# Kernel tuning notes

Hardware: AMD Instinct MI355X
Metric: run time of the kernel (lower is better)

Reference implementation:

```python
import jax, jax.numpy as jnp
import numpy as np
import math

B, S, E, H = 4, 2048, 512, 8
D = E // H

def setup_inputs() -> dict:
    key = jax.random.key(0)
    ks = jax.random.split(key, 12)
    inp = {
        'query': jax.random.normal(ks[0], (B, S, E), jnp.float32),
        'key': jax.random.normal(ks[1], (B, S, E), jnp.float32),
        'value': jax.random.normal(ks[2], (B, S, E), jnp.float32),
        'mask': jnp.ones((B, S), jnp.int32),
        'position_bias': jax.random.normal(ks[3], (H, S, S), jnp.float32) * 0.02,
        'Wq': jax.random.normal(ks[4], (E, E), jnp.float32) * 0.02,
        'bq': jnp.zeros((E,), jnp.float32),
        'Wk': jax.random.normal(ks[5], (E, E), jnp.float32) * 0.02,
        'bk': jnp.zeros((E,), jnp.float32),
        'Wv': jax.random.normal(ks[6], (E, E), jnp.float32) * 0.02,
        'bv': jnp.zeros((E,), jnp.float32),
        'Wo': jax.random.normal(ks[7], (E, E), jnp.float32) * 0.02,
        'bo': jnp.zeros((E,), jnp.float32),
    }
    return inp

def reference(query, key, value, mask, position_bias, Wq, bq, Wk, bk, Wv, bv, Wo, bo):
    scale = math.sqrt(D)
    # torch Linear: x @ W.T + b
    Q = (query @ Wq.T + bq).reshape(B, S, H, D).transpose(0, 2, 1, 3)  # bhsd
    K = (key @ Wk.T + bk).reshape(B, S, H, D).transpose(0, 2, 1, 3)
    V = (value @ Wv.T + bv).reshape(B, S, H, D).transpose(0, 2, 1, 3)
    scores = jnp.einsum('bhqd,bhkd->bhqk', Q, K) / scale
    scores = scores + position_bias[None]
    causal = jnp.triu(jnp.ones((S, S), bool), k=1)  # True above diagonal
    scores = jnp.where(causal[None, None], -jnp.inf, scores)
    scores = jnp.where(mask[:, None, None, :] == 0, -jnp.inf, scores)
    attn = jax.nn.softmax(scores, axis=-1)  # dropout is eval no-op
    ctx = jnp.einsum('bhqk,bhkd->bqhd', attn, V).reshape(B, S, E)
    out = ctx @ Wo.T + bo
    return out, attn
```

## Files before the change

### kernel.cpp

```cpp
#include <hip/hip_runtime.h>

typedef __attribute__((ext_vector_type(8))) __bf16 bf16x8;
typedef __attribute__((ext_vector_type(4))) float f32x4;
typedef __attribute__((ext_vector_type(4))) unsigned short u16x4;
typedef unsigned short u16;

#define OFF_QB   0L
#define OFF_KB   4194304L
#define OFF_VB   8388608L
#define OFF_WQ   12582912L
#define OFF_WK   12845056L
#define OFF_WV   13107200L
#define OFF_WO   13369344L
#define OFF_QS   13631488L
#define OFF_KS   17825792L
#define OFF_VT   22020096L
#define OFF_CTX  26214400L
#define WS_NEEDED_U16 30408704L

static __device__ __forceinline__ u16 f2bf(float f) {
  union { float f; unsigned u; } v; v.f = f;
  unsigned r = v.u + 0x7FFFu + ((v.u >> 16) & 1u);
  return (u16)(r >> 16);
}

static __device__ __forceinline__ f32x4 mfma16(bf16x8 a, bf16x8 b, f32x4 c) {
  return __builtin_amdgcn_mfma_f32_16x16x32_bf16(a, b, c, 0, 0, 0);
}

__global__ __launch_bounds__(256) void k_cvt(
    const float* __restrict__ q, const float* __restrict__ k, const float* __restrict__ v,
    const float* __restrict__ wq, const float* __restrict__ wk, const float* __restrict__ wv,
    const float* __restrict__ wo, u16* __restrict__ ws0) {
  long i = ((long)blockIdx.x * 256 + threadIdx.x) * 4;
  const float* src; u16* dst; long off;
  if (i < 12582912L) {
    int which = (int)(i >> 22); off = i & 4194303L;
    src = which == 0 ? q : which == 1 ? k : v;
    dst = ws0 + (long)which * 4194304L;
  } else {
    long j = i - 12582912L;
    int which = (int)(j >> 18); off = j & 262143L;
    src = which == 0 ? wq : which == 1 ? wk : which == 2 ? wv : wo;
    dst = ws0 + 12582912L + (long)which * 262144L;
  }
  float4 f = *(const float4*)(src + off);
  u16x4 o; o.x = f2bf(f.x); o.y = f2bf(f.y); o.z = f2bf(f.z); o.w = f2bf(f.w);
  *(u16x4*)(dst + off) = o;
}

__global__ __launch_bounds__(256) void k_proj_qk(
    const u16* __restrict__ ws0, const float* __restrict__ bq, const float* __restrict__ bk) {
  const int wv  = threadIdx.x >> 6;
  const int lane = threadIdx.x & 63;
  const int r16 = lane & 15, g8 = (lane >> 4) * 8, rq = (lane >> 4) * 4;
  const int t0 = blockIdx.x * 64 + wv * 16;
  const int e0 = blockIdx.y * 64;
  const int z  = blockIdx.z;
  const u16* xb = ws0 + (z == 0 ? OFF_QB : OFF_KB);
  const u16* wb = ws0 + (z == 0 ? OFF_WQ : OFF_WK);
  const float* bias = (z == 0) ? bq : bk;
  u16* dst = (u16*)ws0 + (z == 0 ? OFF_QS : OFF_KS);
  const float scl = (z == 0) ? 0.125f * 1.4426950408889634f : 1.0f;

  f32x4 acc[4] = {};
  const u16* arow = xb + (long)(t0 + r16) * 512 + g8;
  for (int f = 0; f < 512; f += 32) {
    bf16x8 a = *(const bf16x8*)(arow + f);
#pragma unroll
    for (int nt = 0; nt < 4; ++nt) {
      bf16x8 bfr = *(const bf16x8*)(wb + (long)(e0 + nt * 16 + r16) * 512 + f + g8);
      acc[nt] = mfma16(a, bfr, acc[nt]);
    }
  }
#pragma unroll
  for (int nt = 0; nt < 4; ++nt) {
    int e = e0 + nt * 16 + r16;
    float bb = bias[e];
    int h = e >> 6, d = e & 63;
#pragma unroll
    for (int r = 0; r < 4; ++r) {
      int t = t0 + rq + r;
      int b = t >> 11, s = t & 2047;
      float val = (acc[nt][r] + bb) * scl;
      dst[((long)(b * 8 + h) * 2048 + s) * 64 + d] = f2bf(val);
    }
  }
}

__global__ __launch_bounds__(256) void k_proj_v(
    const u16* __restrict__ ws0, const float* __restrict__ bv) {
  const int wv  = threadIdx.x >> 6;
  const int lane = threadIdx.x & 63;
  const int r16 = lane & 15, g8 = (lane >> 4) * 8, rq = (lane >> 4) * 4;
  const int e0 = blockIdx.x * 64 + wv * 16;
  const int t0 = blockIdx.y * 64;
  const u16* xb = ws0 + OFF_VB;
  const u16* wb = ws0 + OFF_WV;
  u16* vt = (u16*)ws0 + OFF_VT;

  f32x4 acc[4] = {};
  const u16* arow = wb + (long)(e0 + r16) * 512 + g8;
  for (int f = 0; f < 512; f += 32) {
    bf16x8 a = *(const bf16x8*)(arow + f);
#pragma unroll
    for (int nt = 0; nt < 4; ++nt) {
      bf16x8 bfr = *(const bf16x8*)(xb + (long)(t0 + nt * 16 + r16) * 512 + f + g8);
      acc[nt] = mfma16(a, bfr, acc[nt]);
    }
  }
#pragma unroll
  for (int r = 0; r < 4; ++r) {
    int e = e0 + rq + r;
    float bb = bv[e];
    int h = e >> 6, d = e & 63;
#pragma unroll
    for (int nt = 0; nt < 4; ++nt) {
      int t = t0 + nt * 16 + r16;
      int b = t >> 11, s = t & 2047;
      vt[((long)((b * 8 + h) * 64 + d)) * 2048 + s] = f2bf(acc[nt][r] + bb);
    }
  }
}

__global__ __launch_bounds__(256) void k_attn(
    const u16* __restrict__ ws0, const float* __restrict__ pos_bias,
    const int* __restrict__ mask, float* __restrict__ attn_out, u16* __restrict__ ctx) {
  __shared__ float red_l[4][16];
  __shared__ __align__(16) float cred[4][16][68];
  __shared__ __align__(16) float pw[4][16][36];

  const int tid = threadIdx.x;
  const int w = tid >> 6, lane = tid & 63;
  const int r16 = lane & 15, g = lane >> 4;
  const int g8 = g * 8, rq = g * 4;
  const int bh = blockIdx.y;
  const int b = bh >> 3, h = bh & 7;
  const int pair = blockIdx.x;
  const u16* Qs = ws0 + OFF_QS + (long)bh * (2048 * 64);
  const u16* Ks = ws0 + OFF_KS + (long)bh * (2048 * 64);
  const u16* VT = ws0 + OFF_VT + (long)bh * (64 * 2048);
  const int* maskb = mask + b * 2048;
  const float NEG = -1e30f;
  const float L2E = 1.4426950408889634f;
  bool dg[4];
#pragma unroll
  for (int r = 0; r < 4; ++r) dg[r] = (r16 > rq + r);

  for (int qsel = 0; qsel < 2; ++qsel) {
    const int qb = qsel ? (127 - pair) : pair;
    const int q0 = qb * 16;
    const int ntiles = qb + 1;
    bf16x8 qf0 = *(const bf16x8*)(Qs + (long)(q0 + r16) * 64 + g8);
    bf16x8 qf1 = *(const bf16x8*)(Qs + (long)(q0 + r16) * 64 + 32 + g8);
    const float* brow = pos_bias + ((long)h * 2048 + q0 + rq) * 2048;

    float l[4] = {0.f, 0.f, 0.f, 0.f};
    for (int ti = w; ti < ntiles; ti += 4) {
      int kcol = ti * 16 + r16;
      bf16x8 kf0 = *(const bf16x8*)(Ks + (long)kcol * 64 + g8);
      bf16x8 kf1 = *(const bf16x8*)(Ks + (long)kcol * 64 + 32 + g8);
      f32x4 s = {};
      s = mfma16(qf0, kf0, s);
      s = mfma16(qf1, kf1, s);
      bool mz = (maskb[kcol] == 0);
      bool edge = (ti == qb);
#pragma unroll
      for (int r = 0; r < 4; ++r) {
        float sv = fmaf(brow[(long)r * 2048 + kcol], L2E, s[r]);
        if (mz || (edge && dg[r])) sv = NEG;
        l[r] += exp2f(sv);
      }
    }
#pragma unroll
    for (int r = 0; r < 4; ++r)
#pragma unroll
      for (int off = 1; off < 16; off <<= 1) l[r] += __shfl_xor(l[r], off);
    if (r16 == 0) {
#pragma unroll
      for (int r = 0; r < 4; ++r) red_l[w][rq + r] = l[r];
    }
    __syncthreads();
    float cc[4];
#pragma unroll
    for (int r = 0; r < 4; ++r) {
      float ls = red_l[0][rq + r] + red_l[1][rq + r] + red_l[2][rq + r] + red_l[3][rq + r];
      cc[r] = -__log2f(ls);
    }

    f32x4 cacc[4] = {};
    float* arow = attn_out + ((long)bh * 2048 + q0) * 2048;
    for (int ta = 2 * w; ta < ntiles; ta += 8) {
      const int tb = ta + 1;
      const bool have1 = (tb < ntiles);
      {
        int kcol = ta * 16 + r16;
        bf16x8 kf0 = *(const bf16x8*)(Ks + (long)kcol * 64 + g8);
        bf16x8 kf1 = *(const bf16x8*)(Ks + (long)kcol * 64 + 32 + g8);
        f32x4 s = {};
        s = mfma16(qf0, kf0, s);
        s = mfma16(qf1, kf1, s);
        bool mz = (maskb[kcol] == 0);
        bool edge = (ta == qb);
#pragma unroll
        for (int r = 0; r < 4; ++r) {
          float sv = fmaf(brow[(long)r * 2048 + kcol], L2E, s[r]);
          if (mz || (edge && dg[r])) sv = NEG;
          pw[w][rq + r][r16] = exp2f(sv + cc[r]);
        }
      }
      if (have1) {
        int kcol = tb * 16 + r16;
        bf16x8 kf0 = *(const bf16x8*)(Ks + (long)kcol * 64 + g8);
        bf16x8 kf1 = *(const bf16x8*)(Ks + (long)kcol * 64 + 32 + g8);
        f32x4 s = {};
        s = mfma16(qf0, kf0, s);
        s = mfma16(qf1, kf1, s);
        bool mz = (maskb[kcol] == 0);
        bool edge = (tb == qb);
#pragma unroll
        for (int r = 0; r < 4; ++r) {
          float sv = fmaf(brow[(long)r * 2048 + kcol], L2E, s[r]);
          if (mz || (edge && dg[r])) sv = NEG;
          pw[w][rq + r][16 + r16] = exp2f(sv + cc[r]);
        }
      } else {
#pragma unroll
        for (int r = 0; r < 4; ++r) pw[w][rq + r][16 + r16] = 0.0f;
      }
      {
        f32x4 a0 = *(const f32x4*)&pw[w][r16][g8];
        f32x4 a1 = *(const f32x4*)&pw[w][r16][g8 + 4];
        union { bf16x8 v; u16 s[8]; } pu;
#pragma unroll
        for (int j = 0; j < 4; ++j) { pu.s[j] = f2bf(a0[j]); pu.s[4 + j] = f2bf(a1[j]); }
        int tsel = (g < 2) ? ta : (have1 ? tb : ta);
        const u16* vcol = VT + tsel * 16 + (g8 & 15);
#pragma unroll
        for (int dt = 0; dt < 4; ++dt) {
          bf16x8 vf = *(const bf16x8*)(vcol + (long)(dt * 16 + r16) * 2048);
          cacc[dt] = mfma16(pu.v, vf, cacc[dt]);
        }
      }
      {
        int row = lane >> 2, cs = (lane & 3) * 8;
        const float* src = &pw[w][row][cs];
        f32x4 v0 = *(const f32x4*)src;
        f32x4 v1 = *(const f32x4*)(src + 4);
        float* drow = arow + (long)row * 2048 + ta * 16 + cs;
        __builtin_nontemporal_store(v0, (f32x4*)drow);
        __builtin_nontemporal_store(v1, (f32x4*)(drow + 4));
      }
    }
#pragma unroll
    for (int dt = 0; dt < 4; ++dt)
#pragma unroll
      for (int r = 0; r < 4; ++r)
        cred[w][rq + r][dt * 16 + r16] = cacc[dt][r];

    const int tail_start = ((ntiles + 1) & ~1) * 16;
    for (int rr = w; rr < 16; rr += 4) {
      float* rowp = arow + (long)rr * 2048;
      for (int k2 = tail_start + lane * 4; k2 < 2048; k2 += 256) {
        f32x4 z = {0.f, 0.f, 0.f, 0.f};
        __builtin_nontemporal_store(z, (f32x4*)(rowp + k2));
      }
    }
    __syncthreads();
    {
      int row = tid >> 4, c0 = (tid & 15) * 4;
      u16x4 o;
#pragma unroll
      for (int j = 0; j < 4; ++j) {
        float sum = cred[0][row][c0 + j] + cred[1][row][c0 + j] +
                    cred[2][row][c0 + j] + cred[3][row][c0 + j];
        o[j] = f2bf(sum);
      }
      *(u16x4*)&ctx[(long)(b * 2048 + q0 + row) * 512 + h * 64 + c0] = o;
    }
  }
}

__global__ __launch_bounds__(256) void k_oproj(
    const u16* __restrict__ ws0, const float* __restrict__ bo, float* __restrict__ out) {
  const int wv  = threadIdx.x >> 6;
  const int lane = threadIdx.x & 63;
  const int r16 = lane & 15, g8 = (lane >> 4) * 8, rq = (lane >> 4) * 4;
  const int t0 = blockIdx.x * 64 + wv * 16;
  const int e0 = blockIdx.y * 64;
  const u16* ctx = ws0 + OFF_CTX;
  const u16* wb  = ws0 + OFF_WO;
  f32x4 acc[4] = {};
  const u16* arow = ctx + (long)(t0 + r16) * 512 + g8;
  for (int f = 0; f < 512; f += 32) {
    bf16x8 a = *(const bf16x8*)(arow + f);
#pragma unroll
    for (int nt = 0; nt < 4; ++nt) {
      bf16x8 bfr = *(const bf16x8*)(wb + (long)(e0 + nt * 16 + r16) * 512 + f + g8);
      acc[nt] = mfma16(a, bfr, acc[nt]);
    }
  }
#pragma unroll
  for (int nt = 0; nt < 4; ++nt) {
    int e = e0 + nt * 16 + r16;
    float bb = bo[e];
#pragma unroll
    for (int r = 0; r < 4; ++r) {
      out[(long)(t0 + rq + r) * 512 + e] = acc[nt][r] + bb;
    }
  }
}

extern "C" void kernel_launch(void* const* d_in, const int* in_sizes, int n_in,
                              void* d_out, int out_size, void* d_ws, size_t ws_size,
                              hipStream_t stream) {
  if (ws_size < (size_t)WS_NEEDED_U16 * sizeof(u16)) return;
  const float* query = (const float*)d_in[0];
  const float* key   = (const float*)d_in[1];
  const float* value = (const float*)d_in[2];
  const int*   mask  = (const int*)d_in[3];
  const float* pbias = (const float*)d_in[4];
  const float* Wq = (const float*)d_in[5];
  const float* bq = (const float*)d_in[6];
  const float* Wk = (const float*)d_in[7];
  const float* bk = (const float*)d_in[8];
  const float* Wv = (const float*)d_in[9];
  const float* bv = (const float*)d_in[10];
  const float* Wo = (const float*)d_in[11];
  const float* bo = (const float*)d_in[12];
  float* out  = (float*)d_out;
  float* attn = out + 4194304L;
  u16* ws0 = (u16*)d_ws;

  k_cvt<<<13312, 256, 0, stream>>>(query, key, value, Wq, Wk, Wv, Wo, ws0);
  k_proj_qk<<<dim3(128, 8, 2), 256, 0, stream>>>(ws0, bq, bk);
  k_proj_v<<<dim3(8, 128), 256, 0, stream>>>(ws0, bv);
  k_attn<<<dim3(64, 32), 256, 0, stream>>>(ws0, pbias, mask, attn, (u16*)ws0 + OFF_CTX);
  k_oproj<<<dim3(128, 8), 256, 0, stream>>>(ws0, bo, out);
}
```

Baseline: 426.3 us.

## Fuse two-pass softmax into single QK pass with register-cached probabilities

The sum pass and the PV pass are merged. Unnormalized probabilities are computed once, accumulated into P@V, and kept in registers as packed bf16. After the row-sum reduction, the cached values are rescaled by the reciprocal sum and written to the attention output, and the context is normalized at the end. This removes the second QK^T matmul, the second position-bias read and the second exp, but it writes the attention matrix with bf16 precision and uses many registers (64 packed words). It relies on there being no max subtraction, which was already the case.

```diff
diff --git a/kernel.cpp b/kernel.cpp
--- a/kernel.cpp
+++ b/kernel.cpp
@@ -22,6 +22,10 @@
   union { float f; unsigned u; } v; v.f = f;
   unsigned r = v.u + 0x7FFFu + ((v.u >> 16) & 1u);
   return (u16)(r >> 16);
+}
+
+static __device__ __forceinline__ float bf2f(u16 x) {
+  union { unsigned u; float f; } v; v.u = ((unsigned)x) << 16; return v.f;
 }
 
 static __device__ __forceinline__ f32x4 mfma16(bf16x8 a, bf16x8 b, f32x4 c) {
@@ -156,20 +160,72 @@
     const float* brow = pos_bias + ((long)h * 2048 + q0 + rq) * 2048;
 
     float l[4] = {0.f, 0.f, 0.f, 0.f};
-    for (int ti = w; ti < ntiles; ti += 4) {
-      int kcol = ti * 16 + r16;
-      bf16x8 kf0 = *(const bf16x8*)(Ks + (long)kcol * 64 + g8);
-      bf16x8 kf1 = *(const bf16x8*)(Ks + (long)kcol * 64 + 32 + g8);
-      f32x4 s = {};
-      s = mfma16(qf0, kf0, s);
-      s = mfma16(qf1, kf1, s);
-      bool mz = (maskb[kcol] == 0);
-      bool edge = (ti == qb);
-#pragma unroll
-      for (int r = 0; r < 4; ++r) {
-        float sv = fmaf(brow[(long)r * 2048 + kcol], L2E, s[r]);
-        if (mz || (edge && dg[r])) sv = NEG;
-        l[r] += exp2f(sv);
+    f32x4 cacc[4] = {};
+    unsigned pk[16][4];
+#pragma unroll
+    for (int i = 0; i < 16; ++i) {
+      const int ta = 2 * w + 8 * i;
+      if (ta < ntiles) {
+        const int tb = ta + 1;
+        const bool have1 = (tb < ntiles);
+        float p0[4], p1[4];
+        {
+          int kcol = ta * 16 + r16;
+          bf16x8 kf0 = *(const bf16x8*)(Ks + (long)kcol * 64 + g8);
+          bf16x8 kf1 = *(const bf16x8*)(Ks + (long)kcol * 64 + 32 + g8);
+          f32x4 s = {};
+          s = mfma16(qf0, kf0, s);
+          s = mfma16(qf1, kf1, s);
+          bool mz = (maskb[kcol] == 0);
+          bool edge = (ta == qb);
+#pragma unroll
+          for (int r = 0; r < 4; ++r) {
+            float sv = fmaf(brow[(long)r * 2048 + kcol], L2E, s[r]);
+            if (mz || (edge && dg[r])) sv = NEG;
+            p0[r] = exp2f(sv);
+            l[r] += p0[r];
+          }
+        }
+        if (have1) {
+          int kcol = tb * 16 + r16;
+          bf16x8 kf0 = *(const bf16x8*)(Ks + (long)kcol * 64 + g8);
+          bf16x8 kf1 = *(const bf16x8*)(Ks + (long)kcol * 64 + 32 + g8);
+          f32x4 s = {};
+          s = mfma16(qf0, kf0, s);
+          s = mfma16(qf1, kf1, s);
+          bool mz = (maskb[kcol] == 0);
+          bool edge = (tb == qb);
+#pragma unroll
+          for (int r = 0; r < 4; ++r) {
+            float sv = fmaf(brow[(long)r * 2048 + kcol], L2E, s[r]);
+            if (mz || (edge && dg[r])) sv = NEG;
+            p1[r] = exp2f(sv);
+            l[r] += p1[r];
+          }
+        } else {
+#pragma unroll
+          for (int r = 0; r < 4; ++r) p1[r] = 0.0f;
+        }
+#pragma unroll
+        for (int r = 0; r < 4; ++r) {
+          pw[w][rq + r][r16]      = p0[r];
+          pw[w][rq + r][16 + r16] = p1[r];
+          pk[i][r] = (unsigned)f2bf(p0[r]) | ((unsigned)f2bf(p1[r]) << 16);
+        }
+        {
+          f32x4 a0 = *(const f32x4*)&pw[w][r16][g8];
+          f32x4 a1 = *(const f32x4*)&pw[w][r16][g8 + 4];
+          union { bf16x8 v; u16 s_[8]; } pu;
+#pragma unroll
+          for (int j = 0; j < 4; ++j) { pu.s_[j] = f2bf(a0[j]); pu.s_[4 + j] = f2bf(a1[j]); }
+          int tsel = (g < 2) ? ta : (have1 ? tb : ta);
+          const u16* vcol = VT + tsel * 16 + (g8 & 15);
+#pragma unroll
+          for (int dt = 0; dt < 4; ++dt) {
+            bf16x8 vf = *(const bf16x8*)(vcol + (long)(dt * 16 + r16) * 2048);
+            cacc[dt] = mfma16(pu.v, vf, cacc[dt]);
+          }
+        }
       }
     }
 #pragma unroll
@@ -181,75 +237,30 @@
       for (int r = 0; r < 4; ++r) red_l[w][rq + r] = l[r];
     }
     __syncthreads();
-    float cc[4];
+    float ilr[4];
 #pragma unroll
     for (int r = 0; r < 4; ++r) {
       float ls = red_l[0][rq + r] + red_l[1][rq + r] + red_l[2][rq + r] + red_l[3][rq + r];
-      cc[r] = -__log2f(ls);
-    }
-
-    f32x4 cacc[4] = {};
+      ilr[r] = 1.0f / ls;
+    }
+
+    const int wrow = lane >> 2, cs = (lane & 3) * 8;
     float* arow = attn_out + ((long)bh * 2048 + q0) * 2048;
-    for (int ta = 2 * w; ta < ntiles; ta += 8) {
-      const int tb = ta + 1;
-      const bool have1 = (tb < ntiles);
-      {
-        int kcol = ta * 16 + r16;
-        bf16x8 kf0 = *(const bf16x8*)(Ks + (long)kcol * 64 + g8);
-        bf16x8 kf1 = *(const bf16x8*)(Ks + (long)kcol * 64 + 32 + g8);
-        f32x4 s = {};
-        s = mfma16(qf0, kf0, s);
-        s = mfma16(qf1, kf1, s);
-        bool mz = (maskb[kcol] == 0);
-        bool edge = (ta == qb);
+#pragma unroll
+    for (int i = 0; i < 16; ++i) {
+      const int ta = 2 * w + 8 * i;
+      if (ta < ntiles) {
 #pragma unroll
         for (int r = 0; r < 4; ++r) {
-          float sv = fmaf(brow[(long)r * 2048 + kcol], L2E, s[r]);
-          if (mz || (edge && dg[r])) sv = NEG;
-          pw[w][rq + r][r16] = exp2f(sv + cc[r]);
-        }
-      }
-      if (have1) {
-        int kcol = tb * 16 + r16;
-        bf16x8 kf0 = *(const bf16x8*)(Ks + (long)kcol * 64 + g8);
-        bf16x8 kf1 = *(const bf16x8*)(Ks + (long)kcol * 64 + 32 + g8);
-        f32x4 s = {};
-        s = mfma16(qf0, kf0, s);
-        s = mfma16(qf1, kf1, s);
-        bool mz = (maskb[kcol] == 0);
-        bool edge = (tb == qb);
-#pragma unroll
-        for (int r = 0; r < 4; ++r) {
-          float sv = fmaf(brow[(long)r * 2048 + kcol], L2E, s[r]);
-          if (mz || (edge && dg[r])) sv = NEG;
-          pw[w][rq + r][16 + r16] = exp2f(sv + cc[r]);
-        }
-      } else {
-#pragma unroll
-        for (int r = 0; r < 4; ++r) pw[w][rq + r][16 + r16] = 0.0f;
-      }
-      {
-        f32x4 a0 = *(const f32x4*)&pw[w][r16][g8];
-        f32x4 a1 = *(const f32x4*)&pw[w][r16][g8 + 4];
-        union { bf16x8 v; u16 s[8]; } pu;
-#pragma unroll
-        for (int j = 0; j < 4; ++j) { pu.s[j] = f2bf(a0[j]); pu.s[4 + j] = f2bf(a1[j]); }
-        int tsel = (g < 2) ? ta : (have1 ? tb : ta);
-        const u16* vcol = VT + tsel * 16 + (g8 & 15);
-#pragma unroll
-        for (int dt = 0; dt < 4; ++dt) {
-          bf16x8 vf = *(const bf16x8*)(vcol + (long)(dt * 16 + r16) * 2048);
-          cacc[dt] = mfma16(pu.v, vf, cacc[dt]);
-        }
-      }
-      {
-        int row = lane >> 2, cs = (lane & 3) * 8;
-        const float* src = &pw[w][row][cs];
-        f32x4 v0 = *(const f32x4*)src;
-        f32x4 v1 = *(const f32x4*)(src + 4);
-        float* drow = arow + (long)row * 2048 + ta * 16 + cs;
-        __builtin_nontemporal_store(v0, (f32x4*)drow);
-        __builtin_nontemporal_store(v1, (f32x4*)(drow + 4));
+          unsigned v = pk[i][r];
+          pw[w][rq + r][r16]      = bf2f((u16)(v & 0xffffu)) * ilr[r];
+          pw[w][rq + r][16 + r16] = bf2f((u16)(v >> 16)) * ilr[r];
+        }
+        f32x4 v0 = *(const f32x4*)&pw[w][wrow][cs];
+        f32x4 v1 = *(const f32x4*)&pw[w][wrow][cs + 4];
+        float* dp = arow + (long)wrow * 2048 + ta * 16 + cs;
+        __builtin_nontemporal_store(v0, (f32x4*)dp);
+        __builtin_nontemporal_store(v1, (f32x4*)(dp + 4));
       }
     }
 #pragma unroll
@@ -269,15 +280,18 @@
     __syncthreads();
     {
       int row = tid >> 4, c0 = (tid & 15) * 4;
+      float ls2 = red_l[0][row] + red_l[1][row] + red_l[2][row] + red_l[3][row];
+      float il2 = 1.0f / ls2;
       u16x4 o;
 #pragma unroll
       for (int j = 0; j < 4; ++j) {
         float sum = cred[0][row][c0 + j] + cred[1][row][c0 + j] +
                     cred[2][row][c0 + j] + cred[3][row][c0 + j];
-        o[j] = f2bf(sum);
+        o[j] = f2bf(sum * il2);
       }
       *(u16x4*)&ctx[(long)(b * 2048 + q0 + row) * 512 + h * 64 + c0] = o;
     }
+    __syncthreads();
   }
 }
 
```

Result: slower. 655.1 us (+53.7%).
